# Kernel optimization log

Measured on AMD Instinct MI355X. Metric: run time of the kernel, lower is better.

The kernel has to match this reference:

```python
import jax, jax.numpy as jnp
import numpy as np
from jax import lax

HEADS = 8
DIM_HEAD = 64
NUM_LANDMARKS = 256
PINV_ITERS = 6
CONV_PAD = 33 // 2  # 16


def moore_penrose_pinv(x, iters):
    # x: [..., m, m]
    abs_x = jnp.abs(x)
    col = abs_x.sum(-1).max()
    row = abs_x.sum(-2).max()
    z = jnp.swapaxes(x, -1, -2) / (col * row)
    I = jnp.eye(x.shape[-1], dtype=x.dtype)
    for _ in range(iters):
        xz = x @ z
        z = 0.25 * (z @ (13.0 * I - xz @ (15.0 * I - xz @ (7.0 * I - xz))))
    return z


def setup_inputs() -> dict:
    key = jax.random.key(0)
    k1, k2, k3, k4, k5 = jax.random.split(key, 5)
    b, n, dim = 4, 4096, 512
    inner = HEADS * DIM_HEAD
    return {
        "x": jax.random.normal(k1, (b, n, dim), jnp.float32),
        "w_qkv": jax.random.normal(k2, (dim, 3 * inner), jnp.float32) * 0.02,
        "w_out": jax.random.normal(k3, (inner, dim), jnp.float32) * 0.02,
        "b_out": jax.random.normal(k4, (dim,), jnp.float32) * 0.02,
        "res_kernel": jax.random.normal(k5, (HEADS, 1, 33, 1), jnp.float32) * 0.1,
    }


def reference(x, w_qkv, w_out, b_out, res_kernel):
    b, n, dim = x.shape
    h, dh, m = HEADS, DIM_HEAD, NUM_LANDMARKS
    scale = dh ** -0.5
    # n chosen as a multiple of m, so the pad branch is a no-op.
    l = n // m  # tokens per landmark group

    qkv = x @ w_qkv  # [b, n, 3*h*dh]
    q, k, v = jnp.split(qkv, 3, axis=-1)
    to_heads = lambda t: t.reshape(b, n, h, dh).transpose(0, 2, 1, 3)  # [b,h,n,dh]
    q, k, v = to_heads(q), to_heads(k), to_heads(v)
    q = q * scale

    # landmarks: mean over consecutive groups of l tokens
    q_l = q.reshape(b, h, m, l, dh).sum(3) / l  # [b,h,m,dh]
    k_l = k.reshape(b, h, m, l, dh).sum(3) / l

    attn1 = jax.nn.softmax(jnp.einsum("bhnd,bhmd->bhnm", q, k_l), axis=-1)  # [b,h,n,m]
    attn2 = jax.nn.softmax(jnp.einsum("bhid,bhjd->bhij", q_l, k_l), axis=-1)  # [b,h,m,m]
    attn3 = jax.nn.softmax(jnp.einsum("bhmd,bhnd->bhmn", q_l, k), axis=-1)  # [b,h,m,n]

    attn2_pinv = moore_penrose_pinv(attn2, PINV_ITERS)
    out = (attn1 @ attn2_pinv) @ (attn3 @ v)  # [b,h,n,dh]

    # depthwise residual conv over the sequence dim (Conv2d(h, h, (33,1), groups=h))
    res = lax.conv_general_dilated(
        v, res_kernel, window_strides=(1, 1),
        padding=((CONV_PAD, CONV_PAD), (0, 0)),
        dimension_numbers=("NCHW", "OIHW", "NCHW"),
        feature_group_count=h,
    )
    out = out + res

    out = out.transpose(0, 2, 1, 3).reshape(b, n, h * dh)
    out = out @ w_out + b_out
    return out
```

## Files before the change

kernel.cpp:

```cpp
#include <hip/hip_runtime.h>

#define Nq   4096
#define DHq  64
#define Mq   256
#define BHq  32

using bf16 = __bf16;
using bf16x8 = __bf16 __attribute__((ext_vector_type(8)));
using bf16x4 = __bf16 __attribute__((ext_vector_type(4)));
using f32x4 = float __attribute__((ext_vector_type(4)));

__device__ __forceinline__ f32x4 mfma16(bf16x8 a, bf16x8 b, f32x4 c) {
  return __builtin_amdgcn_mfma_f32_16x16x32_bf16(a, b, c, 0, 0, 0);
}
__device__ __forceinline__ unsigned short f2bu(float f) {
  bf16 b = (bf16)f;
  return __builtin_bit_cast(unsigned short, b);
}
__device__ __forceinline__ void split_store(bf16* h, bf16* l, long idx, float v) {
  bf16 hi = (bf16)v;
  h[idx] = hi;
  l[idx] = (bf16)(v - (float)hi);
}

typedef const __attribute__((address_space(1))) void* gas_t;
typedef __attribute__((address_space(3))) void* las_t;
__device__ __forceinline__ void glds16(const bf16* g, bf16* l) {
  __builtin_amdgcn_global_load_lds((gas_t)g, (las_t)l, 16, 0, 0);
}

template<int ROWS, int SRC>
__device__ __forceinline__ void stageA(const void* src, long ld, long row0, int k0,
                                       bf16* dst, int t) {
#pragma unroll
  for (int c = 0; c < ROWS / 64; ++c) {
    int idx = t + 256 * c;
    int r = idx >> 2;
    int kc = (idx & 3) << 3;
    bf16x8 val;
    if constexpr (SRC == 0) {
      val = *(const bf16x8*)((const bf16*)src + (row0 + r) * ld + k0 + kc);
    } else {
      const float* s = (const float*)src + (row0 + r) * ld + k0 + kc;
      float4 a = *(const float4*)s;
      float4 b = *(const float4*)(s + 4);
      val[0]=(bf16)a.x; val[1]=(bf16)a.y; val[2]=(bf16)a.z; val[3]=(bf16)a.w;
      val[4]=(bf16)b.x; val[5]=(bf16)b.y; val[6]=(bf16)b.z; val[7]=(bf16)b.w;
    }
    *(bf16x8*)(dst + r * 40 + kc) = val;
  }
}

template<int COLS, bool F32>
__device__ __forceinline__ void stageBN(const void* src, long ld, long n0, int k0,
                                        unsigned int* dst, int t) {
  int kp = t >> 4;
  int nb = (t & 15) << 2;
#pragma unroll
  for (int g = 0; g < COLS / 64; ++g) {
    int n = nb + (g << 6);
    unsigned int w0, w1, w2, w3;
    if constexpr (F32) {
      const float* s0 = (const float*)src + (long)(k0 + 2 * kp) * ld + n0 + n;
      const float* s1 = s0 + ld;
      float4 a = *(const float4*)s0;
      float4 b = *(const float4*)s1;
      w0 = f2bu(a.x) | ((unsigned)f2bu(b.x) << 16);
      w1 = f2bu(a.y) | ((unsigned)f2bu(b.y) << 16);
      w2 = f2bu(a.z) | ((unsigned)f2bu(b.z) << 16);
      w3 = f2bu(a.w) | ((unsigned)f2bu(b.w) << 16);
    } else {
      const unsigned short* s0 = (const unsigned short*)src + (long)(k0 + 2 * kp) * ld + n0 + n;
      const unsigned short* s1 = s0 + ld;
      ushort4 a = *(const ushort4*)s0;
      ushort4 b = *(const ushort4*)s1;
      w0 = a.x | ((unsigned)b.x << 16);
      w1 = a.y | ((unsigned)b.y << 16);
      w2 = a.z | ((unsigned)b.z << 16);
      w3 = a.w | ((unsigned)b.w << 16);
    }
    dst[(n + 0) * 20 + kp] = w0;
    dst[(n + 1) * 20 + kp] = w1;
    dst[(n + 2) * 20 + kp] = w2;
    dst[(n + 3) * 20 + kp] = w3;
  }
}

#define EQKV 0
#define EA2 1
#define EY 4
#define EWT 8
#define EBIAS 9

struct GP {
  const void* A; const void* Al;
  const void* B; const void* Bl;
  long ldA, ldB, sA, sB;
  int K;
  void* C0; void* C1; void* C2;
  long sC, ldC;
  const void* x0; const void* x1;
  const float* bias;
};

template<int BM, int BN, int WX, int ASRC, int BMODE, int SPLIT, int EPI, int SWZ>
__global__ __launch_bounds__(256, 2) void mgemm(GP p) {
  constexpr int WY = 4 / WX;
  constexpr int TM = BM / WY, TN = BN / WX;
  constexpr int IT = TM / 16, JT = TN / 16;
  constexpr int AB = (SPLIT ? 2 : 1) * BM * 80;
  constexpr int BB = (SPLIT ? 2 : 1) * BN * 80;
  __shared__ __align__(16) char Lbuf[AB + BB];
  bf16* AsL = (bf16*)Lbuf;
  unsigned int* BsL = (unsigned int*)(Lbuf + AB);
  int t = threadIdx.x;
  int wv = t >> 6, lane = t & 63;
  int wy = wv / WX, wx = wv % WX;
  int qd = lane >> 4, lm = lane & 15;
  long bz = blockIdx.z, m0 = (long)blockIdx.y * BM, n0 = (long)blockIdx.x * BN;

  const void* Ap = (const bf16*)p.A + bz * p.sA;
  const void* Alp = nullptr;
  if constexpr (SPLIT) Alp = (const bf16*)p.Al + bz * p.sA;
  const void* Bp = (const bf16*)p.B + bz * p.sB;
  const void* Blp = nullptr;
  if constexpr (SPLIT) Blp = (const bf16*)p.Bl + bz * p.sB;

  f32x4 acc[IT][JT];
#pragma unroll
  for (int i = 0; i < IT; ++i)
#pragma unroll
    for (int j = 0; j < JT; ++j) acc[i][j] = (f32x4)0.0f;

  for (int k0 = 0; k0 < p.K; k0 += 32) {
    stageA<BM, ASRC>(Ap, p.ldA, m0, k0, AsL, t);
    if constexpr (SPLIT) stageA<BM, 0>(Alp, p.ldA, m0, k0, AsL + BM * 40, t);
    if constexpr (BMODE == 0) {
      stageA<BN, 0>(Bp, p.ldB, n0, k0, (bf16*)BsL, t);
      if constexpr (SPLIT) stageA<BN, 0>(Blp, p.ldB, n0, k0, (bf16*)BsL + BN * 40, t);
    } else {
      stageBN<BN, false>(Bp, p.ldB, n0, k0, BsL, t);
      if constexpr (SPLIT) stageBN<BN, false>(Blp, p.ldB, n0, k0, BsL + BN * 20, t);
    }
    __syncthreads();
    bf16x8 af[IT], afl[IT];
#pragma unroll
    for (int i = 0; i < IT; ++i) {
      int m = wy * TM + i * 16 + lm;
      af[i] = *(const bf16x8*)(AsL + m * 40 + qd * 8);
      if constexpr (SPLIT) afl[i] = *(const bf16x8*)(AsL + BM * 40 + m * 40 + qd * 8);
    }
#pragma unroll
    for (int j = 0; j < JT; ++j) {
      int n = wx * TN + j * 16 + lm;
      bf16x8 bf, bfl;
      if constexpr (BMODE == 0) {
        bf = *(const bf16x8*)((const bf16*)BsL + n * 40 + qd * 8);
        if constexpr (SPLIT) bfl = *(const bf16x8*)((const bf16*)BsL + BN * 40 + n * 40 + qd * 8);
      } else {
        bf = *(const bf16x8*)((const bf16*)(BsL + n * 20 + qd * 4));
        if constexpr (SPLIT) bfl = *(const bf16x8*)((const bf16*)(BsL + BN * 20 + n * 20 + qd * 4));
      }
#pragma unroll
      for (int i = 0; i < IT; ++i) {
        acc[i][j] = mfma16(af[i], bf, acc[i][j]);
        if constexpr (SPLIT) {
          acc[i][j] = mfma16(af[i], bfl, acc[i][j]);
          acc[i][j] = mfma16(afl[i], bf, acc[i][j]);
        }
      }
    }
    __syncthreads();
  }

  if constexpr (EPI == EA2) {
#pragma unroll
    for (int r = 0; r < 4; ++r) {
      long row = m0 + wy * TM + qd * 4 + r;
      float e[JT];
      float s = 0.f;
#pragma unroll
      for (int j = 0; j < JT; ++j) { e[j] = __expf(acc[0][j][r]); s += e[j]; }
      s += __shfl_xor(s, 1); s += __shfl_xor(s, 2);
      s += __shfl_xor(s, 4); s += __shfl_xor(s, 8);
      float inv = 1.0f / s;
#pragma unroll
      for (int j = 0; j < JT; ++j) {
        long col = n0 + j * 16 + lm;
        split_store((bf16*)p.C0, (bf16*)p.C1, bz * p.sC + row * p.ldC + col, e[j] * inv);
      }
    }
  } else {
#pragma unroll
    for (int i = 0; i < IT; ++i)
#pragma unroll
      for (int j = 0; j < JT; ++j)
#pragma unroll
        for (int r = 0; r < 4; ++r) {
          long row = m0 + wy * TM + i * 16 + qd * 4 + r;
          long col = n0 + wx * TN + j * 16 + lm;
          float v = acc[i][j][r];
          if constexpr (EPI == EY) {
            split_store((bf16*)p.C0, (bf16*)p.C1, bz * 65536 + row * 256 + col, v);
          } else if constexpr (EPI == EWT) {
            ((bf16*)p.C0)[bz * 16384 + col * 256 + row] = (bf16)v;
          }
        }
  }
}

template<int ASRC, int EPI, int SWZ>
__global__ __launch_bounds__(256, 3) void ggemm(GP p) {
  __shared__ __align__(64) bf16 AsL[128 * 32];
  __shared__ __align__(64) bf16 BsL[128 * 32];
  int t = threadIdx.x, wv = t >> 6, lane = t & 63;
  int wy = wv >> 1, wx = wv & 1;
  int qd = lane >> 4, lm = lane & 15;
  long m0, n0;
  if constexpr (SWZ == 1) {
    int b = blockIdx.x, xcd = b & 7, s = b >> 3;
    m0 = (long)(xcd * 16 + s / 12) * 128; n0 = (long)(s % 12) * 128;
  } else {
    int b = blockIdx.x, xcd = b & 7, s = b >> 3;
    m0 = (long)(xcd * 16 + (s >> 2)) * 128; n0 = (long)(s & 3) * 128;
  }
  const bf16* A = (const bf16*)p.A;
  const bf16* B = (const bf16*)p.B;

  f32x4 acc[4][4];
#pragma unroll
  for (int i = 0; i < 4; ++i)
#pragma unroll
    for (int j = 0; j < 4; ++j) acc[i][j] = (f32x4)0.0f;

  int rsub = lane >> 2;
  int kc = (lane & 3) << 3;
  for (int k0 = 0; k0 < p.K; k0 += 32) {
#pragma unroll
    for (int e = 0; e < 2; ++e) {
      int br = wv * 32 + e * 16;
      long rA = m0 + br + rsub;
      const bf16* gA;
      if constexpr (ASRC == 0) {
        gA = A + rA * p.ldA + k0 + kc;
      } else {
        long bb = rA >> 12, ii = rA & 4095;
        int k = k0 + kc;
        long h = k >> 6, d = k & 63;
        gA = A + (((bb * 8 + h) * 4096 + ii) * 64 + d);
      }
      glds16(gA, AsL + br * 32);
      const bf16* gB = B + (n0 + br + rsub) * p.ldB + k0 + kc;
      glds16(gB, BsL + br * 32);
    }
    __syncthreads();
    bf16x8 af[4];
#pragma unroll
    for (int i = 0; i < 4; ++i)
      af[i] = *(const bf16x8*)(AsL + (wy * 64 + i * 16 + lm) * 32 + qd * 8);
#pragma unroll
    for (int j = 0; j < 4; ++j) {
      bf16x8 bv = *(const bf16x8*)(BsL + (wx * 64 + j * 16 + lm) * 32 + qd * 8);
#pragma unroll
      for (int i = 0; i < 4; ++i) acc[i][j] = mfma16(af[i], bv, acc[i][j]);
    }
    __syncthreads();
  }

#pragma unroll
  for (int i = 0; i < 4; ++i)
#pragma unroll
    for (int j = 0; j < 4; ++j)
#pragma unroll
      for (int r = 0; r < 4; ++r) {
        long row = m0 + wy * 64 + i * 16 + qd * 4 + r;
        long col = n0 + wx * 64 + j * 16 + lm;
        float v = acc[i][j][r];
        if constexpr (EPI == EQKV) {
          int part = (int)(col >> 9);
          long h = (col >> 6) & 7, d = col & 63;
          long bb = row >> 12, ii = row & 4095;
          float scv = part == 0 ? 0.125f : 1.0f;
          bf16* dst = part == 0 ? (bf16*)p.C0 : (part == 1 ? (bf16*)p.C1 : (bf16*)p.C2);
          dst[((bb * 8 + h) * 4096 + ii) * 64 + d] = (bf16)(v * scv);
        } else {
          ((float*)p.C0)[row * 512 + col] = v + p.bias[col];
        }
      }
}

__global__ __launch_bounds__(256) void k_xcast(const float* __restrict__ x,
                                               bf16* __restrict__ xb) {
  long i = ((long)blockIdx.x * 256 + threadIdx.x) * 8;
  float4 a = *(const float4*)(x + i);
  float4 b = *(const float4*)(x + i + 4);
  bf16x8 v;
  v[0]=(bf16)a.x; v[1]=(bf16)a.y; v[2]=(bf16)a.z; v[3]=(bf16)a.w;
  v[4]=(bf16)b.x; v[5]=(bf16)b.y; v[6]=(bf16)b.z; v[7]=(bf16)b.w;
  *(bf16x8*)(xb + i) = v;
}

__global__ __launch_bounds__(256) void k_wtrans(const float* __restrict__ src,
                                                bf16* __restrict__ dst, int N) {
  __shared__ float T[64][65];
  int tj = blockIdx.x, ti = blockIdx.y;
  int t = threadIdx.x;
  int c = t & 63, r0 = t >> 6;
#pragma unroll
  for (int rr = 0; rr < 16; ++rr) {
    int r = r0 * 16 + rr;
    T[r][c] = src[(long)(ti * 64 + r) * N + tj * 64 + c];
  }
  __syncthreads();
#pragma unroll
  for (int rr = 0; rr < 16; ++rr) {
    int n = r0 * 16 + rr;
    dst[(long)(tj * 64 + n) * 512 + ti * 64 + c] = (bf16)T[c][n];
  }
}

#define SBW 132

__device__ __forceinline__ void stageBS(const bf16* src, long n0, int k0,
                                        unsigned int* dst, int t) {
  int kp = t >> 4, nb = (t & 15) << 2;
  const unsigned short* s0 = (const unsigned short*)src + (long)(k0 + 2 * kp) * 256 + n0 + nb;
  const unsigned short* s1 = s0 + 256;
  ushort4 a = *(const ushort4*)s0;
  ushort4 b = *(const ushort4*)s1;
  int wb = (k0 >> 1) + kp;
  dst[(nb + 0) * SBW + wb] = a.x | ((unsigned)b.x << 16);
  dst[(nb + 1) * SBW + wb] = a.y | ((unsigned)b.y << 16);
  dst[(nb + 2) * SBW + wb] = a.z | ((unsigned)b.z << 16);
  dst[(nb + 3) * SBW + wb] = a.w | ((unsigned)b.w << 16);
}

template<int SPLIT>
__device__ __forceinline__ void sgemm(const bf16* Ah, const bf16* Al,
                                      const unsigned int* Bs, const unsigned int* Bsl,
                                      int w, int lane, f32x4 acc[2][4]) {
  int qd = lane >> 4, lm = lane & 15;
#pragma unroll
  for (int i = 0; i < 2; ++i)
#pragma unroll
    for (int j = 0; j < 4; ++j) acc[i][j] = (f32x4)0.0f;
#pragma unroll 2
  for (int k0 = 0; k0 < 256; k0 += 32) {
    bf16x8 af[2], afl[2];
#pragma unroll
    for (int i = 0; i < 2; ++i) {
      long m = w * 32 + i * 16 + lm;
      af[i] = *(const bf16x8*)(Ah + m * 256 + k0 + qd * 8);
      if constexpr (SPLIT) afl[i] = *(const bf16x8*)(Al + m * 256 + k0 + qd * 8);
    }
#pragma unroll
    for (int j = 0; j < 4; ++j) {
      bf16x8 bv = *(const bf16x8*)((const bf16*)(Bs + (j * 16 + lm) * SBW + (k0 >> 1) + qd * 4));
      bf16x8 bl;
      if constexpr (SPLIT)
        bl = *(const bf16x8*)((const bf16*)(Bsl + (j * 16 + lm) * SBW + (k0 >> 1) + qd * 4));
#pragma unroll
      for (int i = 0; i < 2; ++i) {
        acc[i][j] = mfma16(af[i], bv, acc[i][j]);
        if constexpr (SPLIT) {
          acc[i][j] = mfma16(af[i], bl, acc[i][j]);
          acc[i][j] = mfma16(afl[i], bv, acc[i][j]);
        }
      }
    }
  }
}

template<int SPLIT>
__global__ __launch_bounds__(512) void k_nsy(const bf16* __restrict__ A2h,
                                             const bf16* __restrict__ A2l,
                                             const bf16* __restrict__ zh,
                                             const bf16* __restrict__ zl,
                                             bf16* __restrict__ yh, bf16* __restrict__ yl) {
  __shared__ __align__(16) unsigned int Bs[2][64 * SBW];
  int b = blockIdx.x, t = threadIdx.x;
  long bh = b >> 2, js = (long)(b & 3) * 64;
  const bf16* Ah = A2h + bh * 65536;
  const bf16* Al = A2l + bh * 65536;
  const bf16* Bh = zh + bh * 65536;
  const bf16* Bl = zl + bh * 65536;
  if (t < 256) {
#pragma unroll
    for (int k0 = 0; k0 < 256; k0 += 32) {
      stageBS(Bh, js, k0, Bs[0], t);
      if constexpr (SPLIT) stageBS(Bl, js, k0, Bs[1], t);
    }
  }
  __syncthreads();
  int w = t >> 6, lane = t & 63;
  f32x4 acc[2][4];
  sgemm<SPLIT>(Ah, Al, Bs[0], Bs[1], w, lane, acc);
  int qd = lane >> 4, lm = lane & 15;
  bf16* yhb = yh + bh * 65536;
  bf16* ylb = yl + bh * 65536;
#pragma unroll
  for (int i = 0; i < 2; ++i)
#pragma unroll
    for (int j = 0; j < 4; ++j)
#pragma unroll
      for (int r = 0; r < 4; ++r) {
        long row = w * 32 + i * 16 + qd * 4 + r;
        long col = js + j * 16 + lm;
        split_store(yhb, ylb, row * 256 + col, acc[i][j][r]);
      }
}

template<int SPLIT>
__global__ __launch_bounds__(512) void k_ns3(const bf16* __restrict__ yh_,
                                             const bf16* __restrict__ yl_,
                                             const bf16* __restrict__ zh,
                                             const bf16* __restrict__ zl,
                                             bf16* __restrict__ znh, bf16* __restrict__ znl) {
  __shared__ __align__(16) unsigned int S0[2][64 * SBW];
  __shared__ __align__(16) unsigned int S1[2][64 * SBW];
  int b = blockIdx.x, t = threadIdx.x;
  long bh = b >> 2, js = (long)(b & 3) * 64;
  const bf16* yh = yh_ + bh * 65536;
  const bf16* yl = yl_ + bh * 65536;
  const bf16* zch = zh + bh * 65536;
  const bf16* zcl = zl + bh * 65536;
  if (t < 256) {
#pragma unroll
    for (int k0 = 0; k0 < 256; k0 += 32) {
      stageBS(yh, js, k0, S0[0], t);
      if constexpr (SPLIT) stageBS(yl, js, k0, S0[1], t);
    }
  }
  __syncthreads();
  int w = t >> 6, lane = t & 63, qd = lane >> 4, lm = lane & 15;
  f32x4 acc[2][4];

  sgemm<SPLIT>(yh, yl, S0[0], S0[1], w, lane, acc);
#pragma unroll
  for (int i = 0; i < 2; ++i)
#pragma unroll
    for (int j = 0; j < 4; ++j) {
      int R0 = w * 32 + i * 16 + qd * 4;
      int col = j * 16 + lm;
      float v[4];
#pragma unroll
      for (int r = 0; r < 4; ++r) {
        long row = R0 + r;
        long ix = row * 256 + js + col;
        float yv = (float)yh[ix] + (float)yl[ix];
        v[r] = ((row == js + col) ? 15.0f : 0.0f) - 7.0f * yv + acc[i][j][r];
      }
      unsigned int* Wp = S1[0] + col * SBW + (R0 >> 1);
      Wp[0] = f2bu(v[0]) | ((unsigned)f2bu(v[1]) << 16);
      Wp[1] = f2bu(v[2]) | ((unsigned)f2bu(v[3]) << 16);
      if constexpr (SPLIT) {
        unsigned int* Wq = S1[1] + col * SBW + (R0 >> 1);
        Wq[0] = f2bu(v[0] - (float)(bf16)v[0]) | ((unsigned)f2bu(v[1] - (float)(bf16)v[1]) << 16);
        Wq[1] = f2bu(v[2] - (float)(bf16)v[2]) | ((unsigned)f2bu(v[3] - (float)(bf16)v[3]) << 16);
      }
    }
  __syncthreads();

  sgemm<SPLIT>(yh, yl, S1[0], S1[1], w, lane, acc);
#pragma unroll
  for (int i = 0; i < 2; ++i)
#pragma unroll
    for (int j = 0; j < 4; ++j) {
      int R0 = w * 32 + i * 16 + qd * 4;
      int col = j * 16 + lm;
      float v[4];
#pragma unroll
      for (int r = 0; r < 4; ++r)
        v[r] = (((long)(R0 + r) == js + col) ? 13.0f : 0.0f) - acc[i][j][r];
      unsigned int* Wp = S0[0] + col * SBW + (R0 >> 1);
      Wp[0] = f2bu(v[0]) | ((unsigned)f2bu(v[1]) << 16);
      Wp[1] = f2bu(v[2]) | ((unsigned)f2bu(v[3]) << 16);
      if constexpr (SPLIT) {
        unsigned int* Wq = S0[1] + col * SBW + (R0 >> 1);
        Wq[0] = f2bu(v[0] - (float)(bf16)v[0]) | ((unsigned)f2bu(v[1] - (float)(bf16)v[1]) << 16);
        Wq[1] = f2bu(v[2] - (float)(bf16)v[2]) | ((unsigned)f2bu(v[3] - (float)(bf16)v[3]) << 16);
      }
    }
  __syncthreads();

  sgemm<SPLIT>(zch, zcl, S0[0], S0[1], w, lane, acc);
  bf16* zoh = znh + bh * 65536;
  bf16* zol = znl + bh * 65536;
#pragma unroll
  for (int i = 0; i < 2; ++i)
#pragma unroll
    for (int j = 0; j < 4; ++j)
#pragma unroll
      for (int r = 0; r < 4; ++r) {
        long row = w * 32 + i * 16 + qd * 4 + r;
        long col = js + j * 16 + lm;
        split_store(zoh, zol, row * 256 + col, 0.25f * acc[i][j][r]);
      }
}

__global__ __launch_bounds__(256, 2) void k_a3v(const bf16* __restrict__ qlh,
                                                const bf16* __restrict__ kb,
                                                const bf16* __restrict__ vb,
                                                float* __restrict__ a3vf,
                                                float* __restrict__ rs3) {
  __shared__ __align__(16) char L[38400];
  bf16* qlS = (bf16*)L;
  bf16* kS  = (bf16*)(L + 9216);
  bf16* PA  = (bf16*)(L + 18432);
  unsigned int* vB0 = (unsigned int*)(L + 27648);
  unsigned int* vB1 = (unsigned int*)(L + 32768);
  float* rsL = (float*)(L + 37888);
  int b = blockIdx.x, t = threadIdx.x;
  int xcd = b & 7, s = b >> 3;
  int strip = xcd * 16 + (s >> 2);
  int qt = s & 3;
  long bz = strip >> 2;
  int kt = strip & 3;
  int wv = t >> 6, lane = t & 63, qd = lane >> 4, lm = lane & 15;
  int wy = wv >> 1, wx = wv & 1;
  const bf16* qlp = qlh + bz * 16384 + qt * 64 * 64;
#pragma unroll
  for (int c = 0; c < 2; ++c) {
    int idx = t + 256 * c;
    int r = idx >> 3, dc = (idx & 7) * 8;
    *(bf16x8*)(qlS + r * 72 + dc) = *(const bf16x8*)(qlp + r * 64 + dc);
  }
  const bf16* kb_ = kb + bz * 262144 + (long)kt * 65536;
  const bf16* vb_ = vb + bz * 262144 + (long)kt * 65536;
  f32x4 accO[2][2];
  float rsum[2][4];
#pragma unroll
  for (int i = 0; i < 2; ++i) {
#pragma unroll
    for (int j = 0; j < 2; ++j) accO[i][j] = (f32x4)0.0f;
#pragma unroll
    for (int r = 0; r < 4; ++r) rsum[i][r] = 0.f;
  }
  for (int tt = 0; tt < 16; ++tt) {
    __syncthreads();
    const bf16* ks_ = kb_ + tt * 4096;
#pragma unroll
    for (int c = 0; c < 2; ++c) {
      int idx = t + 256 * c;
      int r = idx >> 3, dc = (idx & 7) * 8;
      *(bf16x8*)(kS + r * 72 + dc) = *(const bf16x8*)(ks_ + r * 64 + dc);
    }
    const bf16* vs_ = vb_ + tt * 4096;
    stageBN<64, false>(vs_, 64, 0, 0, vB0, t);
    stageBN<64, false>(vs_, 64, 0, 32, vB1, t);
    __syncthreads();
    f32x4 s2[2][2];
#pragma unroll
    for (int i = 0; i < 2; ++i)
#pragma unroll
      for (int j = 0; j < 2; ++j) s2[i][j] = (f32x4)0.0f;
#pragma unroll
    for (int ks = 0; ks < 2; ++ks) {
      bf16x8 af[2], bfv[2];
#pragma unroll
      for (int i = 0; i < 2; ++i)
        af[i] = *(const bf16x8*)(qlS + (wy * 32 + i * 16 + lm) * 72 + ks * 32 + qd * 8);
#pragma unroll
      for (int j = 0; j < 2; ++j)
        bfv[j] = *(const bf16x8*)(kS + (wx * 32 + j * 16 + lm) * 72 + ks * 32 + qd * 8);
#pragma unroll
      for (int i = 0; i < 2; ++i)
#pragma unroll
        for (int j = 0; j < 2; ++j) s2[i][j] = mfma16(af[i], bfv[j], s2[i][j]);
    }
#pragma unroll
    for (int i = 0; i < 2; ++i)
#pragma unroll
      for (int r = 0; r < 4; ++r) {
        float e0 = __expf(s2[i][0][r]);
        float e1 = __expf(s2[i][1][r]);
        int row = wy * 32 + i * 16 + qd * 4 + r;
        PA[row * 72 + wx * 32 + 0 * 16 + lm] = (bf16)e0;
        PA[row * 72 + wx * 32 + 1 * 16 + lm] = (bf16)e1;
        float cs = e0 + e1;
        cs += __shfl_xor(cs, 1); cs += __shfl_xor(cs, 2);
        cs += __shfl_xor(cs, 4); cs += __shfl_xor(cs, 8);
        rsum[i][r] += cs;
      }
    __syncthreads();
#pragma unroll
    for (int ks = 0; ks < 2; ++ks) {
      unsigned int* vB = ks ? vB1 : vB0;
      bf16x8 af[2], bfv[2];
#pragma unroll
      for (int i = 0; i < 2; ++i)
        af[i] = *(const bf16x8*)(PA + (wy * 32 + i * 16 + lm) * 72 + ks * 32 + qd * 8);
#pragma unroll
      for (int j = 0; j < 2; ++j)
        bfv[j] = *(const bf16x8*)((const bf16*)(vB + (wx * 32 + j * 16 + lm) * 20) + qd * 8);
#pragma unroll
      for (int i = 0; i < 2; ++i)
#pragma unroll
        for (int j = 0; j < 2; ++j) accO[i][j] = mfma16(af[i], bfv[j], accO[i][j]);
    }
  }
  if (lm == 0) {
#pragma unroll
    for (int i = 0; i < 2; ++i)
#pragma unroll
      for (int r = 0; r < 4; ++r)
        rsL[(wy * 32 + i * 16 + qd * 4 + r) * 2 + wx] = rsum[i][r];
  }
  __syncthreads();
  if (t < 64) atomicAdd(&rs3[bz * 256 + qt * 64 + t], rsL[t * 2] + rsL[t * 2 + 1]);
#pragma unroll
  for (int i = 0; i < 2; ++i)
#pragma unroll
    for (int j = 0; j < 2; ++j)
#pragma unroll
      for (int r = 0; r < 4; ++r) {
        long row = bz * 256 + qt * 64 + wy * 32 + i * 16 + qd * 4 + r;
        long col = wx * 32 + j * 16 + lm;
        atomicAdd(&a3vf[row * 64 + col], accO[i][j][r]);
      }
}

__global__ void k_a3vnorm(const float* __restrict__ a3vf, const float* __restrict__ rs3,
                          bf16* __restrict__ a3vh, bf16* __restrict__ a3vl) {
  long e0 = ((long)blockIdx.x * 256 + threadIdx.x) * 4;
  float4 vv = *(const float4*)&a3vf[e0];
  float inv = 1.0f / rs3[e0 >> 6];
  split_store(a3vh, a3vl, e0 + 0, vv.x * inv);
  split_store(a3vh, a3vl, e0 + 1, vv.y * inv);
  split_store(a3vh, a3vl, e0 + 2, vv.z * inv);
  split_store(a3vh, a3vl, e0 + 3, vv.w * inv);
}

__global__ void k_zero(float* a3vf, float* rs3, unsigned int* sc) {
  long i = (long)blockIdx.x * 256 + threadIdx.x;
  a3vf[i] = 0.f;
  if (i < 8192) rs3[i] = 0.f;
  if (i == 0) sc[0] = 0u;
}

__global__ void k_landmarks(const bf16* q, const bf16* k, bf16* qlh, bf16* qll,
                            bf16* klh, bf16* kll) {
  int bm = blockIdx.x;
  int bh = bm >> 8, mi = bm & 255;
  int d = threadIdx.x;
  const bf16* qp = q + ((long)bh * 4096 + mi * 16) * 64 + d;
  const bf16* kp = k + ((long)bh * 4096 + mi * 16) * 64 + d;
  float sq = 0.f, sk = 0.f;
#pragma unroll
  for (int tt = 0; tt < 16; ++tt) { sq += (float)qp[tt * 64]; sk += (float)kp[tt * 64]; }
  sq *= 0.0625f; sk *= 0.0625f;
  long o = (long)bh * 16384 + mi * 64 + d;
  split_store(qlh, qll, o, sq);
  split_store(klh, kll, o, sk);
}

__global__ __launch_bounds__(256) void k_colsum(const bf16* A2h, const bf16* A2l,
                                                unsigned int* sc) {
  int bh = blockIdx.x, j = threadIdx.x;
  const bf16* ph = A2h + (long)bh * 65536 + j;
  const bf16* pl = A2l + (long)bh * 65536 + j;
  float s = 0.f;
  for (int i = 0; i < 256; ++i) s += (float)ph[i * 256] + (float)pl[i * 256];
  __shared__ float red[256];
  red[j] = s; __syncthreads();
  for (int o = 128; o > 0; o >>= 1) {
    if (j < o) red[j] = fmaxf(red[j], red[j + o]);
    __syncthreads();
  }
  if (j == 0) atomicMax(sc, __float_as_uint(red[0]));
}

__global__ __launch_bounds__(256) void k_zinit(const bf16* A2h, const bf16* A2l,
                                               const unsigned int* sc, bf16* zh, bf16* zl) {
  __shared__ float T[64][65];
  int bh = blockIdx.z, ti = blockIdx.y, tj = blockIdx.x;
  int t = threadIdx.x;
  int c = t & 63, r0 = t >> 6;
  long base = (long)bh * 65536;
  float inv = 1.0f / __uint_as_float(sc[0]);
#pragma unroll
  for (int rr = 0; rr < 16; ++rr) {
    int r = r0 * 16 + rr;
    long idx = base + (long)(ti * 64 + r) * 256 + tj * 64 + c;
    T[r][c] = (float)A2h[idx] + (float)A2l[idx];
  }
  __syncthreads();
#pragma unroll
  for (int rr = 0; rr < 16; ++rr) {
    int jl = r0 * 16 + rr;
    float v = T[c][jl] * inv;
    long o = base + (long)(tj * 64 + jl) * 256 + ti * 64 + c;
    split_store(zh, zl, o, v);
  }
}

__global__ __launch_bounds__(256, 2) void k_attn1w(const bf16* qb, const bf16* klb,
                                                   const bf16* Wt, bf16* oh) {
  __shared__ __align__(16) char L[38912];
  bf16* Aq = (bf16*)L;
  bf16* Bkl = (bf16*)(L + 5120);
  bf16* Pl = (bf16*)L;
  bf16* Bw = (bf16*)(L + 33792);
  int t = threadIdx.x, wv = t >> 6, lane = t & 63;
  int qd = lane >> 4, lm = lane & 15;
  long bz = blockIdx.z;
  long m0 = (long)blockIdx.x * 64;
  const bf16* qA = qb + bz * (4096L * 64);
  const bf16* klA = klb + bz * (256L * 64);
  const bf16* WtA = Wt + bz * 16384;

  f32x4 a1[16];
#pragma unroll
  for (int j = 0; j < 16; ++j) a1[j] = (f32x4)0.0f;
  for (int k0 = 0; k0 < 64; k0 += 32) {
    stageA<64, 0>(qA, 64, m0, k0, Aq, t);
    stageA<256, 0>(klA, 64, 0, k0, Bkl, t);
    __syncthreads();
    bf16x8 af = *(const bf16x8*)(Aq + (wv * 16 + lm) * 40 + qd * 8);
#pragma unroll
    for (int j = 0; j < 16; ++j) {
      bf16x8 bf = *(const bf16x8*)(Bkl + (j * 16 + lm) * 40 + qd * 8);
      a1[j] = mfma16(af, bf, a1[j]);
    }
    __syncthreads();
  }
  float rs[4];
#pragma unroll
  for (int r = 0; r < 4; ++r) {
    int rowl = wv * 16 + qd * 4 + r;
    float ev[16];
    float s = 0.f;
#pragma unroll
    for (int j = 0; j < 16; ++j) { ev[j] = __expf(a1[j][r]); s += ev[j]; }
    s += __shfl_xor(s, 1); s += __shfl_xor(s, 2);
    s += __shfl_xor(s, 4); s += __shfl_xor(s, 8);
    rs[r] = s;
#pragma unroll
    for (int j = 0; j < 16; ++j) {
      float other = __shfl_xor(ev[j], 1);
      if ((lm & 1) == 0) {
        unsigned int w = f2bu(ev[j]) | ((unsigned)f2bu(other) << 16);
        *(unsigned int*)(Pl + rowl * 264 + j * 16 + lm) = w;
      }
    }
  }
  f32x4 a2[4];
#pragma unroll
  for (int j = 0; j < 4; ++j) a2[j] = (f32x4)0.0f;
  for (int k0 = 0; k0 < 256; k0 += 32) {
    stageA<64, 0>(WtA, 256, 0, k0, Bw, t);
    __syncthreads();
    bf16x8 af = *(const bf16x8*)(Pl + (wv * 16 + lm) * 264 + k0 + qd * 8);
#pragma unroll
    for (int j = 0; j < 4; ++j) {
      bf16x8 bf = *(const bf16x8*)(Bw + (j * 16 + lm) * 40 + qd * 8);
      a2[j] = mfma16(af, bf, a2[j]);
    }
    __syncthreads();
  }
#pragma unroll
  for (int j = 0; j < 4; ++j)
#pragma unroll
    for (int r = 0; r < 4; ++r) {
      long grow = m0 + wv * 16 + qd * 4 + r;
      long col = j * 16 + lm;
      oh[(bz * 4096 + grow) * 64 + col] = (bf16)(a2[j][r] / rs[r]);
    }
}

__global__ __launch_bounds__(256) void k_conv2(const bf16* __restrict__ v,
                                               const float* __restrict__ kern,
                                               bf16* __restrict__ oh) {
  __shared__ __align__(16) bf16 Vs[96 * 72];
  int bx = blockIdx.x;
  int bh = bx >> 6;
  int i0 = (bx & 63) * 64;
  int t = threadIdx.x;
  const bf16* vsrc = v + (long)bh * 262144;
#pragma unroll
  for (int c = 0; c < 3; ++c) {
    int idx = t + 256 * c;
    int r = idx >> 3, dc = (idx & 7) * 8;
    int grow = i0 + r - 16;
    bf16x8 val = (bf16x8)(bf16)0.0f;
    if (grow >= 0 && grow < 4096) val = *(const bf16x8*)(vsrc + (long)grow * 64 + dc);
    *(bf16x8*)(Vs + r * 72 + dc) = val;
  }
  __syncthreads();
  int dg = t & 15, rg = t >> 4;
  const float* kc = kern + (bh & 7) * 33;
  float acc[4][4] = {};
#pragma unroll
  for (int rr = 0; rr < 36; ++rr) {
    bf16x4 xv = *(const bf16x4*)(Vs + (rg * 4 + rr) * 72 + dg * 4);
    float x0 = (float)xv[0], x1 = (float)xv[1], x2 = (float)xv[2], x3 = (float)xv[3];
#pragma unroll
    for (int r = 0; r < 4; ++r) {
      int u = rr - r;
      if (u >= 0 && u < 33) {
        float kw = kc[u];
        acc[r][0] = fmaf(kw, x0, acc[r][0]);
        acc[r][1] = fmaf(kw, x1, acc[r][1]);
        acc[r][2] = fmaf(kw, x2, acc[r][2]);
        acc[r][3] = fmaf(kw, x3, acc[r][3]);
      }
    }
  }
  long base = ((long)bh * 4096 + i0 + rg * 4) * 64 + dg * 4;
#pragma unroll
  for (int r = 0; r < 4; ++r) {
    bf16x4 o = *(const bf16x4*)(oh + base + r * 64);
    bf16x4 w;
#pragma unroll
    for (int c = 0; c < 4; ++c) w[c] = (bf16)(acc[r][c] + (float)o[c]);
    *(bf16x4*)(oh + base + r * 64) = w;
  }
}

extern "C" void kernel_launch(void* const* d_in, const int* in_sizes, int n_in,
                              void* d_out, int out_size, void* d_ws, size_t ws_size,
                              hipStream_t stream) {
  const float* x     = (const float*)d_in[0];
  const float* w_qkv = (const float*)d_in[1];
  const float* w_out = (const float*)d_in[2];
  const float* b_out = (const float*)d_in[3];
  const float* res_k = (const float*)d_in[4];

  char* w = (char*)d_ws;
  bf16* qb  = (bf16*)(w);
  bf16* kb  = (bf16*)(w + 16777216);
  bf16* vb  = (bf16*)(w + 33554432);
  bf16* qlh = (bf16*)(w + 50331648);
  bf16* qll = (bf16*)(w + 51380224);
  bf16* klh = (bf16*)(w + 52428800);
  bf16* kll = (bf16*)(w + 53477376);
  bf16* A2h = (bf16*)(w + 54525952);
  bf16* A2l = (bf16*)(w + 58720256);
  bf16* zAh = (bf16*)(w + 62914560);
  bf16* zAl = (bf16*)(w + 67108864);
  bf16* zBh = (bf16*)(w + 71303168);
  bf16* zBl = (bf16*)(w + 75497472);
  bf16* yh  = (bf16*)(w + 79691776);
  bf16* yl  = (bf16*)(w + 83886080);
  bf16* wqt = (bf16*)(w + 88080384);
  bf16* wot = (bf16*)(w + 89653248);
  bf16* oh  = (bf16*)(w + 104857600);
  bf16* xb  = (bf16*)(w + 104857600);
  float* a3vf = (float*)(w + 121634816);
  bf16* a3vh = (bf16*)(w + 123731968);
  bf16* a3vl = (bf16*)(w + 124780544);
  bf16* Wt   = (bf16*)(w + 125829120);
  float* rs3 = (float*)(w + 126877696);
  unsigned int* sc  = (unsigned int*)(w + 126910464);

  k_zero<<<2048, 256, 0, stream>>>(a3vf, rs3, sc);

  k_xcast<<<4096, 256, 0, stream>>>(x, xb);
  k_wtrans<<<dim3(24, 8), 256, 0, stream>>>(w_qkv, wqt, 1536);
  k_wtrans<<<dim3(8, 8), 256, 0, stream>>>(w_out, wot, 512);

  GP p{};
  p.A = xb; p.ldA = 512; p.B = wqt; p.ldB = 512; p.K = 512;
  p.C0 = qb; p.C1 = kb; p.C2 = vb;
  ggemm<0, EQKV, 1><<<1536, 256, 0, stream>>>(p);

  k_landmarks<<<8192, 64, 0, stream>>>(qb, kb, qlh, qll, klh, kll);

  p = GP{};
  p.A = qlh; p.Al = qll; p.ldA = 64; p.sA = 16384;
  p.B = klh; p.Bl = kll; p.ldB = 64; p.sB = 16384; p.K = 64;
  p.C0 = A2h; p.C1 = A2l; p.sC = 65536; p.ldC = 256;
  mgemm<64, 256, 1, 0, 0, 1, EA2, 0><<<dim3(1, 4, 32), 256, 0, stream>>>(p);

  k_colsum<<<32, 256, 0, stream>>>(A2h, A2l, sc);
  k_zinit<<<dim3(4, 4, 32), 256, 0, stream>>>(A2h, A2l, sc, zAh, zAl);

  k_a3v<<<512, 256, 0, stream>>>(qlh, kb, vb, a3vf, rs3);
  k_a3vnorm<<<512, 256, 0, stream>>>(a3vf, rs3, a3vh, a3vl);

  bf16 *zch = zAh, *zcl = zAl, *znh = zBh, *znl = zBl;
  for (int it = 0; it < 6; ++it) {
    if (it < 4) {
      k_nsy<0><<<128, 512, 0, stream>>>(A2h, A2l, zch, zcl, yh, yl);
      k_ns3<0><<<128, 512, 0, stream>>>(yh, yl, zch, zcl, znh, znl);
    } else {
      k_nsy<1><<<128, 512, 0, stream>>>(A2h, A2l, zch, zcl, yh, yl);
      k_ns3<1><<<128, 512, 0, stream>>>(yh, yl, zch, zcl, znh, znl);
    }
    bf16* tmp;
    tmp = zch; zch = znh; znh = tmp;
    tmp = zcl; zcl = znl; znl = tmp;
  }

  p = GP{};
  p.A = zch; p.Al = zcl; p.ldA = 256; p.sA = 65536;
  p.B = a3vh; p.Bl = a3vl; p.ldB = 64; p.sB = 16384; p.K = 256;
  p.C0 = Wt;
  mgemm<64, 64, 2, 0, 1, 1, EWT, 0><<<dim3(1, 4, 32), 256, 0, stream>>>(p);

  k_attn1w<<<dim3(64, 1, 32), 256, 0, stream>>>(qb, klh, Wt, oh);

  k_conv2<<<2048, 256, 0, stream>>>(vb, res_k, oh);

  p = GP{};
  p.A = oh; p.ldA = 64; p.B = wot; p.ldB = 512; p.K = 512;
  p.C0 = d_out; p.bias = b_out;
  ggemm<3, EBIAS, 2><<<512, 256, 0, stream>>>(p);
}
```

Baseline: 509.4 us.

## Fuse Newton-Schulz y=A·z into previous step and halve column strips

The pinv iteration now computes the next step's A2·z product at the end of each step kernel, dropping a separate k_nsy launch per iteration; only the first product uses a standalone kernel. Column strips shrink from 64 to 32 so 256 blocks are launched instead of 128, improving CU occupancy on the small batched 256x256 matmuls. The zeroing kernel is merged into the x cast kernel, and the two weight transposes are merged into one launch. In exchange each fused step kernel reads the A operand once more per extra strip and keeps double y buffers in the workspace.

```diff
diff --git a/kernel.cpp b/kernel.cpp
--- a/kernel.cpp
+++ b/kernel.cpp
@@ -88,7 +88,6 @@
 
 #define EQKV 0
 #define EA2 1
-#define EY 4
 #define EWT 8
 #define EBIAS 9
 
@@ -200,9 +199,7 @@
           long row = m0 + wy * TM + i * 16 + qd * 4 + r;
           long col = n0 + wx * TN + j * 16 + lm;
           float v = acc[i][j][r];
-          if constexpr (EPI == EY) {
-            split_store((bf16*)p.C0, (bf16*)p.C1, bz * 65536 + row * 256 + col, v);
-          } else if constexpr (EPI == EWT) {
+          if constexpr (EPI == EWT) {
             ((bf16*)p.C0)[bz * 16384 + col * 256 + row] = (bf16)v;
           }
         }
@@ -289,21 +286,31 @@
       }
 }
 
-__global__ __launch_bounds__(256) void k_xcast(const float* __restrict__ x,
-                                               bf16* __restrict__ xb) {
-  long i = ((long)blockIdx.x * 256 + threadIdx.x) * 8;
-  float4 a = *(const float4*)(x + i);
-  float4 b = *(const float4*)(x + i + 4);
+__global__ __launch_bounds__(256) void k_prep(const float* __restrict__ x,
+                                              bf16* __restrict__ xb,
+                                              float* a3vf, float* rs3, unsigned int* sc) {
+  long i = (long)blockIdx.x * 256 + threadIdx.x;
+  long e = i * 8;
+  float4 a = *(const float4*)(x + e);
+  float4 b = *(const float4*)(x + e + 4);
   bf16x8 v;
   v[0]=(bf16)a.x; v[1]=(bf16)a.y; v[2]=(bf16)a.z; v[3]=(bf16)a.w;
   v[4]=(bf16)b.x; v[5]=(bf16)b.y; v[6]=(bf16)b.z; v[7]=(bf16)b.w;
-  *(bf16x8*)(xb + i) = v;
-}
-
-__global__ __launch_bounds__(256) void k_wtrans(const float* __restrict__ src,
-                                                bf16* __restrict__ dst, int N) {
+  *(bf16x8*)(xb + e) = v;
+  if (i < 524288) a3vf[i] = 0.f;
+  if (i < 8192) rs3[i] = 0.f;
+  if (i == 0) sc[0] = 0u;
+}
+
+__global__ __launch_bounds__(256) void k_wtrans2(const float* __restrict__ wq,
+                                                 const float* __restrict__ wo,
+                                                 bf16* __restrict__ wqt,
+                                                 bf16* __restrict__ wot) {
   __shared__ float T[64][65];
-  int tj = blockIdx.x, ti = blockIdx.y;
+  int bx = blockIdx.x, ti = blockIdx.y;
+  const float* src; bf16* dst; int N, tj;
+  if (bx < 24) { src = wq; dst = wqt; N = 1536; tj = bx; }
+  else         { src = wo; dst = wot; N = 512;  tj = bx - 24; }
   int t = threadIdx.x;
   int c = t & 63, r0 = t >> 6;
 #pragma unroll
@@ -321,9 +328,9 @@
 
 #define SBW 132
 
-__device__ __forceinline__ void stageBS(const bf16* src, long n0, int k0,
-                                        unsigned int* dst, int t) {
-  int kp = t >> 4, nb = (t & 15) << 2;
+__device__ __forceinline__ void stageBS32(const bf16* src, long n0, int k0,
+                                          unsigned int* dst, int t) {
+  int kp = t >> 3, nb = (t & 7) << 2;
   const unsigned short* s0 = (const unsigned short*)src + (long)(k0 + 2 * kp) * 256 + n0 + nb;
   const unsigned short* s1 = s0 + 256;
   ushort4 a = *(const ushort4*)s0;
@@ -336,14 +343,14 @@
 }
 
 template<int SPLIT>
-__device__ __forceinline__ void sgemm(const bf16* Ah, const bf16* Al,
-                                      const unsigned int* Bs, const unsigned int* Bsl,
-                                      int w, int lane, f32x4 acc[2][4]) {
+__device__ __forceinline__ void sgemm32(const bf16* Ah, const bf16* Al,
+                                        const unsigned int* Bs, const unsigned int* Bsl,
+                                        int w, int lane, f32x4 acc[2][2]) {
   int qd = lane >> 4, lm = lane & 15;
 #pragma unroll
   for (int i = 0; i < 2; ++i)
 #pragma unroll
-    for (int j = 0; j < 4; ++j) acc[i][j] = (f32x4)0.0f;
+    for (int j = 0; j < 2; ++j) acc[i][j] = (f32x4)0.0f;
 #pragma unroll 2
   for (int k0 = 0; k0 < 256; k0 += 32) {
     bf16x8 af[2], afl[2];
@@ -354,7 +361,7 @@
       if constexpr (SPLIT) afl[i] = *(const bf16x8*)(Al + m * 256 + k0 + qd * 8);
     }
 #pragma unroll
-    for (int j = 0; j < 4; ++j) {
+    for (int j = 0; j < 2; ++j) {
       bf16x8 bv = *(const bf16x8*)((const bf16*)(Bs + (j * 16 + lm) * SBW + (k0 >> 1) + qd * 4));
       bf16x8 bl;
       if constexpr (SPLIT)
@@ -371,37 +378,41 @@
   }
 }
 
-template<int SPLIT>
-__global__ __launch_bounds__(512) void k_nsy(const bf16* __restrict__ A2h,
-                                             const bf16* __restrict__ A2l,
-                                             const bf16* __restrict__ zh,
-                                             const bf16* __restrict__ zl,
-                                             bf16* __restrict__ yh, bf16* __restrict__ yl) {
-  __shared__ __align__(16) unsigned int Bs[2][64 * SBW];
+template<int HASL>
+__device__ __forceinline__ void packStrip(unsigned int* Sh, unsigned int* Sl,
+                                          int col, int R0, const float* v) {
+  unsigned int* Wp = Sh + col * SBW + (R0 >> 1);
+  Wp[0] = f2bu(v[0]) | ((unsigned)f2bu(v[1]) << 16);
+  Wp[1] = f2bu(v[2]) | ((unsigned)f2bu(v[3]) << 16);
+  if constexpr (HASL) {
+    unsigned int* Wq = Sl + col * SBW + (R0 >> 1);
+    Wq[0] = f2bu(v[0] - (float)(bf16)v[0]) | ((unsigned)f2bu(v[1] - (float)(bf16)v[1]) << 16);
+    Wq[1] = f2bu(v[2] - (float)(bf16)v[2]) | ((unsigned)f2bu(v[3] - (float)(bf16)v[3]) << 16);
+  }
+}
+
+__global__ __launch_bounds__(512) void k_nsy0(const bf16* __restrict__ A2h,
+                                              const bf16* __restrict__ zh,
+                                              bf16* __restrict__ yh, bf16* __restrict__ yl) {
+  __shared__ __align__(16) unsigned int Bs[32 * SBW];
   int b = blockIdx.x, t = threadIdx.x;
-  long bh = b >> 2, js = (long)(b & 3) * 64;
+  long bh = b >> 3, js = (long)(b & 7) * 32;
   const bf16* Ah = A2h + bh * 65536;
-  const bf16* Al = A2l + bh * 65536;
-  const bf16* Bh = zh + bh * 65536;
-  const bf16* Bl = zl + bh * 65536;
-  if (t < 256) {
-#pragma unroll
-    for (int k0 = 0; k0 < 256; k0 += 32) {
-      stageBS(Bh, js, k0, Bs[0], t);
-      if constexpr (SPLIT) stageBS(Bl, js, k0, Bs[1], t);
-    }
+  const bf16* Bz = zh + bh * 65536;
+  if (t < 128) {
+#pragma unroll
+    for (int k0 = 0; k0 < 256; k0 += 32) stageBS32(Bz, js, k0, Bs, t);
   }
   __syncthreads();
-  int w = t >> 6, lane = t & 63;
-  f32x4 acc[2][4];
-  sgemm<SPLIT>(Ah, Al, Bs[0], Bs[1], w, lane, acc);
-  int qd = lane >> 4, lm = lane & 15;
+  int w = t >> 6, lane = t & 63, qd = lane >> 4, lm = lane & 15;
+  f32x4 acc[2][2];
+  sgemm32<0>(Ah, Ah, Bs, Bs, w, lane, acc);
   bf16* yhb = yh + bh * 65536;
   bf16* ylb = yl + bh * 65536;
 #pragma unroll
   for (int i = 0; i < 2; ++i)
 #pragma unroll
-    for (int j = 0; j < 4; ++j)
+    for (int j = 0; j < 2; ++j)
 #pragma unroll
       for (int r = 0; r < 4; ++r) {
         long row = w * 32 + i * 16 + qd * 4 + r;
@@ -410,36 +421,43 @@
       }
 }
 
-template<int SPLIT>
-__global__ __launch_bounds__(512) void k_ns3(const bf16* __restrict__ yh_,
-                                             const bf16* __restrict__ yl_,
-                                             const bf16* __restrict__ zh,
-                                             const bf16* __restrict__ zl,
-                                             bf16* __restrict__ znh, bf16* __restrict__ znl) {
-  __shared__ __align__(16) unsigned int S0[2][64 * SBW];
-  __shared__ __align__(16) unsigned int S1[2][64 * SBW];
+template<int SPLIT, int YS>
+__global__ __launch_bounds__(512) void k_ns4(
+    const bf16* __restrict__ A2h, const bf16* __restrict__ A2l,
+    const bf16* __restrict__ yih, const bf16* __restrict__ yil,
+    const bf16* __restrict__ zh_, const bf16* __restrict__ zl_,
+    bf16* __restrict__ znh_, bf16* __restrict__ znl_,
+    bf16* __restrict__ yoh_, bf16* __restrict__ yol_) {
+  constexpr int P0 = SPLIT ? 2 : 1;
+  constexpr int P1 = (SPLIT || YS == 1) ? 2 : 1;
+  __shared__ __align__(16) unsigned int S0[P0][32 * SBW];
+  __shared__ __align__(16) unsigned int S1[P1][32 * SBW];
   int b = blockIdx.x, t = threadIdx.x;
-  long bh = b >> 2, js = (long)(b & 3) * 64;
-  const bf16* yh = yh_ + bh * 65536;
-  const bf16* yl = yl_ + bh * 65536;
-  const bf16* zch = zh + bh * 65536;
-  const bf16* zcl = zl + bh * 65536;
-  if (t < 256) {
+  long bh = b >> 3, js = (long)(b & 7) * 32;
+  const bf16* yH = yih + bh * 65536;
+  const bf16* yL = yil + bh * 65536;
+  const bf16* zH = zh_ + bh * 65536;
+  const bf16* zL = zl_ + bh * 65536;
+  const bf16* aH = A2h + bh * 65536;
+  const bf16* aL = A2l + bh * 65536;
+  unsigned int* S0l = S0[P0 - 1];
+  unsigned int* S1l = S1[P1 - 1];
+  if (t < 128) {
 #pragma unroll
     for (int k0 = 0; k0 < 256; k0 += 32) {
-      stageBS(yh, js, k0, S0[0], t);
-      if constexpr (SPLIT) stageBS(yl, js, k0, S0[1], t);
+      stageBS32(yH, js, k0, S0[0], t);
+      if constexpr (SPLIT) stageBS32(yL, js, k0, S0l, t);
     }
   }
   __syncthreads();
   int w = t >> 6, lane = t & 63, qd = lane >> 4, lm = lane & 15;
-  f32x4 acc[2][4];
-
-  sgemm<SPLIT>(yh, yl, S0[0], S0[1], w, lane, acc);
+  f32x4 acc[2][2];
+
+  sgemm32<SPLIT>(yH, yL, S0[0], S0l, w, lane, acc);
 #pragma unroll
   for (int i = 0; i < 2; ++i)
 #pragma unroll
-    for (int j = 0; j < 4; ++j) {
+    for (int j = 0; j < 2; ++j) {
       int R0 = w * 32 + i * 16 + qd * 4;
       int col = j * 16 + lm;
       float v[4];
@@ -447,55 +465,62 @@
       for (int r = 0; r < 4; ++r) {
         long row = R0 + r;
         long ix = row * 256 + js + col;
-        float yv = (float)yh[ix] + (float)yl[ix];
+        float yv = (float)yH[ix] + (float)yL[ix];
         v[r] = ((row == js + col) ? 15.0f : 0.0f) - 7.0f * yv + acc[i][j][r];
       }
-      unsigned int* Wp = S1[0] + col * SBW + (R0 >> 1);
-      Wp[0] = f2bu(v[0]) | ((unsigned)f2bu(v[1]) << 16);
-      Wp[1] = f2bu(v[2]) | ((unsigned)f2bu(v[3]) << 16);
-      if constexpr (SPLIT) {
-        unsigned int* Wq = S1[1] + col * SBW + (R0 >> 1);
-        Wq[0] = f2bu(v[0] - (float)(bf16)v[0]) | ((unsigned)f2bu(v[1] - (float)(bf16)v[1]) << 16);
-        Wq[1] = f2bu(v[2] - (float)(bf16)v[2]) | ((unsigned)f2bu(v[3] - (float)(bf16)v[3]) << 16);
-      }
+      packStrip<SPLIT>(S1[0], S1l, col, R0, v);
     }
   __syncthreads();
 
-  sgemm<SPLIT>(yh, yl, S1[0], S1[1], w, lane, acc);
+  sgemm32<SPLIT>(yH, yL, S1[0], S1l, w, lane, acc);
 #pragma unroll
   for (int i = 0; i < 2; ++i)
 #pragma unroll
-    for (int j = 0; j < 4; ++j) {
+    for (int j = 0; j < 2; ++j) {
       int R0 = w * 32 + i * 16 + qd * 4;
       int col = j * 16 + lm;
       float v[4];
 #pragma unroll
       for (int r = 0; r < 4; ++r)
         v[r] = (((long)(R0 + r) == js + col) ? 13.0f : 0.0f) - acc[i][j][r];
-      unsigned int* Wp = S0[0] + col * SBW + (R0 >> 1);
-      Wp[0] = f2bu(v[0]) | ((unsigned)f2bu(v[1]) << 16);
-      Wp[1] = f2bu(v[2]) | ((unsigned)f2bu(v[3]) << 16);
-      if constexpr (SPLIT) {
-        unsigned int* Wq = S0[1] + col * SBW + (R0 >> 1);
-        Wq[0] = f2bu(v[0] - (float)(bf16)v[0]) | ((unsigned)f2bu(v[1] - (float)(bf16)v[1]) << 16);
-        Wq[1] = f2bu(v[2] - (float)(bf16)v[2]) | ((unsigned)f2bu(v[3] - (float)(bf16)v[3]) << 16);
-      }
+      packStrip<SPLIT>(S0[0], S0l, col, R0, v);
     }
   __syncthreads();
 
-  sgemm<SPLIT>(zch, zcl, S0[0], S0[1], w, lane, acc);
-  bf16* zoh = znh + bh * 65536;
-  bf16* zol = znl + bh * 65536;
+  sgemm32<SPLIT>(zH, zL, S0[0], S0l, w, lane, acc);
+  bf16* zoh = znh_ + bh * 65536;
+  bf16* zol = znl_ + bh * 65536;
 #pragma unroll
   for (int i = 0; i < 2; ++i)
 #pragma unroll
-    for (int j = 0; j < 4; ++j)
+    for (int j = 0; j < 2; ++j) {
+      int R0 = w * 32 + i * 16 + qd * 4;
+      int col = j * 16 + lm;
+      float v[4];
 #pragma unroll
       for (int r = 0; r < 4; ++r) {
-        long row = w * 32 + i * 16 + qd * 4 + r;
-        long col = js + j * 16 + lm;
-        split_store(zoh, zol, row * 256 + col, 0.25f * acc[i][j][r]);
-      }
+        v[r] = 0.25f * acc[i][j][r];
+        split_store(zoh, zol, (long)(R0 + r) * 256 + js + col, v[r]);
+      }
+      if constexpr (YS >= 0) packStrip<(YS == 1) ? 1 : 0>(S1[0], S1l, col, R0, v);
+    }
+
+  if constexpr (YS >= 0) {
+    __syncthreads();
+    sgemm32<(YS == 1) ? 1 : 0>(aH, aL, S1[0], S1l, w, lane, acc);
+    bf16* yoh = yoh_ + bh * 65536;
+    bf16* yol = yol_ + bh * 65536;
+#pragma unroll
+    for (int i = 0; i < 2; ++i)
+#pragma unroll
+      for (int j = 0; j < 2; ++j)
+#pragma unroll
+        for (int r = 0; r < 4; ++r) {
+          long row = w * 32 + i * 16 + qd * 4 + r;
+          long col = js + j * 16 + lm;
+          split_store(yoh, yol, row * 256 + col, acc[i][j][r]);
+        }
+  }
 }
 
 __global__ __launch_bounds__(256, 2) void k_a3v(const bf16* __restrict__ qlh,
@@ -631,13 +656,6 @@
   split_store(a3vh, a3vl, e0 + 3, vv.w * inv);
 }
 
-__global__ void k_zero(float* a3vf, float* rs3, unsigned int* sc) {
-  long i = (long)blockIdx.x * 256 + threadIdx.x;
-  a3vf[i] = 0.f;
-  if (i < 8192) rs3[i] = 0.f;
-  if (i == 0) sc[0] = 0u;
-}
-
 __global__ void k_landmarks(const bf16* q, const bf16* k, bf16* qlh, bf16* qll,
                             bf16* klh, bf16* kll) {
   int bm = blockIdx.x;
@@ -844,6 +862,8 @@
   bf16* yl  = (bf16*)(w + 83886080);
   bf16* wqt = (bf16*)(w + 88080384);
   bf16* wot = (bf16*)(w + 89653248);
+  bf16* y2h = (bf16*)(w + 96468992);
+  bf16* y2l = (bf16*)(w + 100663296);
   bf16* oh  = (bf16*)(w + 104857600);
   bf16* xb  = (bf16*)(w + 104857600);
   float* a3vf = (float*)(w + 121634816);
@@ -853,11 +873,8 @@
   float* rs3 = (float*)(w + 126877696);
   unsigned int* sc  = (unsigned int*)(w + 126910464);
 
-  k_zero<<<2048, 256, 0, stream>>>(a3vf, rs3, sc);
-
-  k_xcast<<<4096, 256, 0, stream>>>(x, xb);
-  k_wtrans<<<dim3(24, 8), 256, 0, stream>>>(w_qkv, wqt, 1536);
-  k_wtrans<<<dim3(8, 8), 256, 0, stream>>>(w_out, wot, 512);
+  k_prep<<<4096, 256, 0, stream>>>(x, xb, a3vf, rs3, sc);
+  k_wtrans2<<<dim3(32, 8), 256, 0, stream>>>(w_qkv, w_out, wqt, wot);
 
   GP p{};
   p.A = xb; p.ldA = 512; p.B = wqt; p.ldB = 512; p.K = 512;
@@ -878,18 +895,23 @@
   k_a3v<<<512, 256, 0, stream>>>(qlh, kb, vb, a3vf, rs3);
   k_a3vnorm<<<512, 256, 0, stream>>>(a3vf, rs3, a3vh, a3vl);
 
+  k_nsy0<<<256, 512, 0, stream>>>(A2h, zAh, yh, yl);
   bf16 *zch = zAh, *zcl = zAl, *znh = zBh, *znl = zBl;
+  bf16 *yih = yh, *yil = yl, *yoh = y2h, *yol = y2l;
   for (int it = 0; it < 6; ++it) {
-    if (it < 4) {
-      k_nsy<0><<<128, 512, 0, stream>>>(A2h, A2l, zch, zcl, yh, yl);
-      k_ns3<0><<<128, 512, 0, stream>>>(yh, yl, zch, zcl, znh, znl);
-    } else {
-      k_nsy<1><<<128, 512, 0, stream>>>(A2h, A2l, zch, zcl, yh, yl);
-      k_ns3<1><<<128, 512, 0, stream>>>(yh, yl, zch, zcl, znh, znl);
-    }
+    if (it < 3)
+      k_ns4<0, 0><<<256, 512, 0, stream>>>(A2h, A2l, yih, yil, zch, zcl, znh, znl, yoh, yol);
+    else if (it == 3)
+      k_ns4<0, 1><<<256, 512, 0, stream>>>(A2h, A2l, yih, yil, zch, zcl, znh, znl, yoh, yol);
+    else if (it == 4)
+      k_ns4<1, 1><<<256, 512, 0, stream>>>(A2h, A2l, yih, yil, zch, zcl, znh, znl, yoh, yol);
+    else
+      k_ns4<1, -1><<<256, 512, 0, stream>>>(A2h, A2l, yih, yil, zch, zcl, znh, znl, yoh, yol);
     bf16* tmp;
     tmp = zch; zch = znh; znh = tmp;
     tmp = zcl; zcl = znl; znl = tmp;
+    tmp = yih; yih = yoh; yoh = tmp;
+    tmp = yil; yil = yol; yol = tmp;
   }
 
   p = GP{};
```

Result: faster. 482.1 us (-5.4%).
